# Kernel tuning notes

Hardware: AMD Instinct MI355X
Metric: run time of the kernel (lower is better)

The kernel has to match this reference:

```python
import jax, jax.numpy as jnp
import numpy as np

V, E, S_MAX, H, L = 32000, 1024, 2048, 16, 6
D = E // H  # head_dim = 64
EPS = 1e-5


def _ln(x, g, b):
    mu = jnp.mean(x, axis=-1, keepdims=True)
    var = jnp.mean(jnp.square(x - mu), axis=-1, keepdims=True)
    return (x - mu) * jax.lax.rsqrt(var + EPS) * g + b


def setup_inputs() -> dict:
    key = jax.random.key(0)
    ks = iter(jax.random.split(key, 32))
    std = 0.02
    B, S = 1, 2048
    inp = {
        "tokens": jax.random.randint(next(ks), (B, S), 0, V, dtype=jnp.int32),
        "W_emb": jax.random.normal(next(ks), (V, E), jnp.float32) * std,  # tied with fc_out
        "W_pos": jax.random.normal(next(ks), (S_MAX, E), jnp.float32) * std,
        # per-layer stacked params [L, ...]
        "Wq": jax.random.normal(next(ks), (L, E, E), jnp.float32) * std,
        "Wk": jax.random.normal(next(ks), (L, E, E), jnp.float32) * std,
        "Wv": jax.random.normal(next(ks), (L, E, E), jnp.float32) * std,
        "Wo": jax.random.normal(next(ks), (L, E, E), jnp.float32) * std,
        "bo": jnp.zeros((L, E), jnp.float32),
        "ln1_g": jnp.ones((L, E), jnp.float32),
        "ln1_b": jnp.zeros((L, E), jnp.float32),
        "ln2_g": jnp.ones((L, E), jnp.float32),
        "ln2_b": jnp.zeros((L, E), jnp.float32),
        "W1": jax.random.normal(next(ks), (L, 4 * E, E), jnp.float32) * std,
        "b1": jnp.zeros((L, 4 * E), jnp.float32),
        "W2": jax.random.normal(next(ks), (L, E, 4 * E), jnp.float32) * std,
        "b2": jnp.zeros((L, E), jnp.float32),
        "lnf_g": jnp.ones((E,), jnp.float32),
        "lnf_b": jnp.zeros((E,), jnp.float32),
    }
    return inp


def _gpt_forward(tokens, W_emb, W_pos, Wq, Wk, Wv, Wo, bo, ln1_g, ln1_b,
                 ln2_g, ln2_b, W1, b1, W2, b2, lnf_g, lnf_b):
    B, S = tokens.shape
    x = W_emb[tokens] + W_pos[:S][None, :, :]  # [B,S,E]
    causal = jnp.tril(jnp.ones((S, S), bool))  # [S,S]
    scale = 1.0 / np.sqrt(D)

    def block(x, p):
        wq, wk, wv, wo, bo_, g1, b1n, g2, b2n, w1, bf1, w2, bf2 = p
        h = _ln(x, g1, b1n)
        # torch Linear: y = x @ W.T ; split heads -> [B,H,S,D]
        def heads(w):
            return (h @ w.T).reshape(B, S, H, D).transpose(0, 2, 1, 3)
        q, k, v = heads(wq), heads(wk), heads(wv)
        scores = jnp.einsum('bhqd,bhkd->bhqk', q, k) * scale
        scores = jnp.where(causal[None, None], scores, -jnp.inf)
        attn = jax.nn.softmax(scores, axis=-1)
        o = jnp.einsum('bhqk,bhkd->bhqd', attn, v)
        o = o.transpose(0, 2, 1, 3).reshape(B, S, E)
        x = x + o @ wo.T + bo_
        h2 = _ln(x, g2, b2n)
        ff = jax.nn.gelu(h2 @ w1.T + bf1, approximate=False) @ w2.T + bf2
        return x + ff, None

    params = (Wq, Wk, Wv, Wo, bo, ln1_g, ln1_b, ln2_g, ln2_b, W1, b1, W2, b2)
    x, _ = jax.lax.scan(block, x, params)
    x = _ln(x, lnf_g, lnf_b)
    return x @ W_emb.T  # tied output projection [B,S,V]


def reference(tokens, W_emb, W_pos, Wq, Wk, Wv, Wo, bo, ln1_g, ln1_b,
              ln2_g, ln2_b, W1, b1, W2, b2, lnf_g, lnf_b):
    return _gpt_forward(tokens, W_emb, W_pos, Wq, Wk, Wv, Wo, bo, ln1_g,
                        ln1_b, ln2_g, ln2_b, W1, b1, W2, b2, lnf_g, lnf_b)
```

## Files before the change

kernel.cpp:

```cpp
#include <hip/hip_runtime.h>
#include <math.h>

#define S_LEN 2048
#define EMB 1024
#define NHEAD 16
#define HDIM 64
#define NLAYER 6
#define VOCAB 32000
#define FFDIM 4096

using f32x4 = __attribute__((ext_vector_type(4))) float;
using bf16x8 = __attribute__((ext_vector_type(8))) __bf16;
typedef unsigned short us;

static __device__ __forceinline__ unsigned short f2bf(float f) {
  union { float f; unsigned int u; } v; v.f = f;
  unsigned int r = v.u + 0x7FFFu + ((v.u >> 16) & 1u);
  return (unsigned short)(r >> 16);
}

#define GLOAD_LDS16(g, l)                                                      \
  __builtin_amdgcn_global_load_lds(                                            \
      (const __attribute__((address_space(1))) void*)(g),                      \
      (__attribute__((address_space(3))) void*)(l), 16, 0, 0)

__global__ __launch_bounds__(256) void cvt_bf16_kernel(
    const float* __restrict__ in, us* __restrict__ out, long n) {
  long i = ((long)blockIdx.x * 256 + threadIdx.x) * 8;
  if (i >= n) return;
  const float4* p = (const float4*)(in + i);
  float4 a = p[0], b = p[1];
  uint4 o;
  o.x = (unsigned)f2bf(a.x) | ((unsigned)f2bf(a.y) << 16);
  o.y = (unsigned)f2bf(a.z) | ((unsigned)f2bf(a.w) << 16);
  o.z = (unsigned)f2bf(b.x) | ((unsigned)f2bf(b.y) << 16);
  o.w = (unsigned)f2bf(b.z) | ((unsigned)f2bf(b.w) << 16);
  *(uint4*)(out + i) = o;
}

__global__ __launch_bounds__(256) void embed_kernel(
    const int* __restrict__ tok, const float* __restrict__ Wemb,
    const float* __restrict__ Wpos, float* __restrict__ x) {
  int s = blockIdx.x, t = threadIdx.x;
  int tk = tok[s];
  const float4* we = (const float4*)(Wemb + (size_t)tk * EMB);
  const float4* wp = (const float4*)(Wpos + (size_t)s * EMB);
  float4 a = we[t], b = wp[t];
  float4 o; o.x = a.x + b.x; o.y = a.y + b.y; o.z = a.z + b.z; o.w = a.w + b.w;
  ((float4*)(x + (size_t)s * EMB))[t] = o;
}

__global__ __launch_bounds__(256) void ln_kernel(
    const float* __restrict__ x, const float* __restrict__ g,
    const float* __restrict__ b, us* __restrict__ out) {
  int row = blockIdx.x, t = threadIdx.x, lane = t & 63, wave = t >> 6;
  float4 v = ((const float4*)(x + (size_t)row * EMB))[t];
  float s = v.x + v.y + v.z + v.w;
  float q = v.x * v.x + v.y * v.y + v.z * v.z + v.w * v.w;
  #pragma unroll
  for (int d = 1; d < 64; d <<= 1) { s += __shfl_xor(s, d); q += __shfl_xor(q, d); }
  __shared__ float rs[4], rq[4];
  if (lane == 0) { rs[wave] = s; rq[wave] = q; }
  __syncthreads();
  s = rs[0] + rs[1] + rs[2] + rs[3];
  q = rq[0] + rq[1] + rq[2] + rq[3];
  float mean = s * (1.0f / EMB);
  float var = q * (1.0f / EMB) - mean * mean;
  float rstd = rsqrtf(var + 1e-5f);
  float4 gg = ((const float4*)g)[t], bb = ((const float4*)b)[t];
  ushort4 o;
  o.x = f2bf((v.x - mean) * rstd * gg.x + bb.x);
  o.y = f2bf((v.y - mean) * rstd * gg.y + bb.y);
  o.z = f2bf((v.z - mean) * rstd * gg.z + bb.z);
  o.w = f2bf((v.w - mean) * rstd * gg.w + bb.w);
  ((ushort4*)(out + (size_t)row * EMB))[t] = o;
}

template <int HAS_BIAS, int HAS_RES, int DO_GELU, int OUT_BF16>
__global__ __launch_bounds__(256) void gemm_bb(
    const us* __restrict__ A, const us* __restrict__ B0,
    const us* __restrict__ B1, const us* __restrict__ B2,
    const float* __restrict__ bias, const float* __restrict__ res,
    void* C0, void* C1, void* C2, int M, int N, int K) {
  const us* B = blockIdx.z == 0 ? B0 : (blockIdx.z == 1 ? B1 : B2);
  void* C = blockIdx.z == 0 ? C0 : (blockIdx.z == 1 ? C1 : C2);
  const int nwg = gridDim.x * gridDim.y;
  int lin = blockIdx.y * gridDim.x + blockIdx.x;
  {
    const int qx = nwg >> 3, r = nwg & 7;
    const int xcd = lin & 7, idx = lin >> 3;
    lin = (xcd < r ? xcd * (qx + 1) : r * (qx + 1) + (xcd - r) * qx) + idx;
  }
  const int m0 = (lin % gridDim.x) * 128, n0 = (lin / gridDim.x) * 128;
  const int t = threadIdx.x, lane = t & 63, wave = t >> 6;
  const int wm = (wave >> 1) * 64, wn = (wave & 1) * 64;
  __shared__ __align__(16) us As[128 * 64];
  __shared__ __align__(16) us Bs[128 * 64];
  f32x4 acc[4][4] = {};
  const int kIters = K >> 6;
  const int cbase = wave * 64;
  const int myc = cbase + lane;
  for (int kt = 0; kt < kIters; ++kt) {
    const int k0 = kt << 6;
    __syncthreads();
    #pragma unroll
    for (int i = 0; i < 4; ++i) {
      const int c = myc + i * 256;
      const int row = c >> 3, col = (c & 7) * 8;
      GLOAD_LDS16(A + (size_t)(m0 + row) * K + k0 + col,
                  As + (size_t)(cbase + i * 256) * 8);
    }
    #pragma unroll
    for (int i = 0; i < 4; ++i) {
      const int c = myc + i * 256;
      const int row = c >> 3, col = (c & 7) * 8;
      GLOAD_LDS16(B + (size_t)(n0 + row) * K + k0 + col,
                  Bs + (size_t)(cbase + i * 256) * 8);
    }
    __syncthreads();
    #pragma unroll
    for (int ks = 0; ks < 2; ++ks) {
      bf16x8 af[4], bfr[4];
      #pragma unroll
      for (int i = 0; i < 4; ++i)
        af[i] = *(const bf16x8*)(As + (wm + i * 16 + (lane & 15)) * 64 + ks * 32 + (lane >> 4) * 8);
      #pragma unroll
      for (int j = 0; j < 4; ++j)
        bfr[j] = *(const bf16x8*)(Bs + (wn + j * 16 + (lane & 15)) * 64 + ks * 32 + (lane >> 4) * 8);
      #pragma unroll
      for (int i = 0; i < 4; ++i)
        #pragma unroll
        for (int j = 0; j < 4; ++j)
          acc[i][j] = __builtin_amdgcn_mfma_f32_16x16x32_bf16(af[i], bfr[j], acc[i][j], 0, 0, 0);
    }
  }
  const int r0 = (lane >> 4) * 4, cl = lane & 15;
  #pragma unroll
  for (int i = 0; i < 4; ++i) {
    #pragma unroll
    for (int j = 0; j < 4; ++j) {
      const int col = n0 + wn + j * 16 + cl;
      float bv = HAS_BIAS ? bias[col] : 0.0f;
      #pragma unroll
      for (int r = 0; r < 4; ++r) {
        const int row = m0 + wm + i * 16 + r0 + r;
        float val = acc[i][j][r] + bv;
        if (DO_GELU) val = val * 0.5f * (1.0f + erff(val * 0.70710678118f));
        if (HAS_RES) val += res[(size_t)row * N + col];
        if (OUT_BF16) ((us*)C)[(size_t)row * N + col] = f2bf(val);
        else          ((float*)C)[(size_t)row * N + col] = val;
      }
    }
  }
}

__global__ __launch_bounds__(256) void gemm_sk(
    const us* __restrict__ A, const us* __restrict__ B,
    float* __restrict__ C, int M, int N, int K, int kSlice) {
  const int z = blockIdx.z;
  const int nwg = gridDim.x * gridDim.y;
  int lin = blockIdx.y * gridDim.x + blockIdx.x;
  {
    const int qx = nwg >> 3, r = nwg & 7;
    const int xcd = lin & 7, idx = lin >> 3;
    lin = (xcd < r ? xcd * (qx + 1) : r * (qx + 1) + (xcd - r) * qx) + idx;
  }
  const int m0 = (lin % gridDim.x) * 128, n0 = (lin / gridDim.x) * 128;
  const int t = threadIdx.x, lane = t & 63, wave = t >> 6;
  const int wm = (wave >> 1) * 64, wn = (wave & 1) * 64;
  __shared__ __align__(16) us As[128 * 64];
  __shared__ __align__(16) us Bs[128 * 64];
  f32x4 acc[4][4] = {};
  const int cbase = wave * 64;
  const int myc = cbase + lane;
  const int kBeg = z * kSlice;
  const int kIters = kSlice >> 6;
  for (int kt = 0; kt < kIters; ++kt) {
    const int k0 = kBeg + (kt << 6);
    __syncthreads();
    #pragma unroll
    for (int i = 0; i < 4; ++i) {
      const int c = myc + i * 256;
      const int row = c >> 3, col = (c & 7) * 8;
      GLOAD_LDS16(A + (size_t)(m0 + row) * K + k0 + col,
                  As + (size_t)(cbase + i * 256) * 8);
    }
    #pragma unroll
    for (int i = 0; i < 4; ++i) {
      const int c = myc + i * 256;
      const int row = c >> 3, col = (c & 7) * 8;
      GLOAD_LDS16(B + (size_t)(n0 + row) * K + k0 + col,
                  Bs + (size_t)(cbase + i * 256) * 8);
    }
    __syncthreads();
    #pragma unroll
    for (int ks = 0; ks < 2; ++ks) {
      bf16x8 af[4], bfr[4];
      #pragma unroll
      for (int i = 0; i < 4; ++i)
        af[i] = *(const bf16x8*)(As + (wm + i * 16 + (lane & 15)) * 64 + ks * 32 + (lane >> 4) * 8);
      #pragma unroll
      for (int j = 0; j < 4; ++j)
        bfr[j] = *(const bf16x8*)(Bs + (wn + j * 16 + (lane & 15)) * 64 + ks * 32 + (lane >> 4) * 8);
      #pragma unroll
      for (int i = 0; i < 4; ++i)
        #pragma unroll
        for (int j = 0; j < 4; ++j)
          acc[i][j] = __builtin_amdgcn_mfma_f32_16x16x32_bf16(af[i], bfr[j], acc[i][j], 0, 0, 0);
    }
  }
  float* Cz = C + (size_t)z * M * N;
  const int r0 = (lane >> 4) * 4, cl = lane & 15;
  #pragma unroll
  for (int i = 0; i < 4; ++i)
    #pragma unroll
    for (int j = 0; j < 4; ++j) {
      const int col = n0 + wn + j * 16 + cl;
      #pragma unroll
      for (int r = 0; r < 4; ++r)
        Cz[(size_t)(m0 + wm + i * 16 + r0 + r) * N + col] = acc[i][j][r];
    }
}

template <int SK>
__global__ __launch_bounds__(256) void reduce_sk_kernel(
    float* __restrict__ x, const float* __restrict__ p,
    const float* __restrict__ bias) {
  const size_t i = ((size_t)blockIdx.x * 256 + threadIdx.x) * 4;
  const size_t plane = (size_t)S_LEN * EMB;
  float4 v = *(const float4*)(x + i);
  float4 b = *(const float4*)(bias + (i & (EMB - 1)));
  v.x += b.x; v.y += b.y; v.z += b.z; v.w += b.w;
  #pragma unroll
  for (int z = 0; z < SK; ++z) {
    float4 q = *(const float4*)(p + z * plane + i);
    v.x += q.x; v.y += q.y; v.z += q.z; v.w += q.w;
  }
  *(float4*)(x + i) = v;
}

__global__ __launch_bounds__(256) void attn_kernel(
    const us* __restrict__ qb, const us* __restrict__ kb,
    const us* __restrict__ vb, us* __restrict__ ob) {
  const int qt = gridDim.x - 1 - blockIdx.x;
  const int head = blockIdx.y;
  const int t = threadIdx.x, lane = t & 63, wave = t >> 6;
  const int hi = lane >> 4, lq = lane & 15;
  const int hd = head * HDIM;
  const int q0w = qt * 64 + wave * 16;
  __shared__ __align__(16) us Kl[64 * 64];
  __shared__ __align__(16) us Vl[64][72];
  __shared__ __align__(16) us Pl[4][16][72];
  bf16x8 qf[2];
  {
    const us* qp = qb + (size_t)(q0w + lq) * EMB + hd + hi * 8;
    qf[0] = *(const bf16x8*)qp;
    qf[1] = *(const bf16x8*)(qp + 32);
  }
  f32x4 accO[4] = {};
  float m_run = -1e30f, l_run = 0.f;
  const int vr = t >> 2, vd = (t & 3) * 16;
  const int q_g = q0w + lq;
  for (int kt = 0; kt <= qt; ++kt) {
    __syncthreads();
    #pragma unroll
    for (int i = 0; i < 2; ++i) {
      const int c = wave * 64 + lane + i * 256;
      const int row = c >> 3, j = c & 7;
      const int colE = (j * 8) ^ ((row & 7) << 3);
      GLOAD_LDS16(kb + (size_t)(kt * 64 + row) * EMB + hd + colE,
                  Kl + (size_t)(wave * 64 + i * 256) * 8);
    }
    {
      const us* vp = vb + (size_t)(kt * 64 + vr) * EMB + hd + vd;
      uint4 a = *(const uint4*)vp;
      uint4 b = *(const uint4*)(vp + 8);
      unsigned int w[8] = {a.x, a.y, a.z, a.w, b.x, b.y, b.z, b.w};
      #pragma unroll
      for (int i = 0; i < 8; ++i) {
        Vl[vd + 2 * i][vr] = (us)(w[i] & 0xffffu);
        Vl[vd + 2 * i + 1][vr] = (us)(w[i] >> 16);
      }
    }
    __syncthreads();
    f32x4 sc[4] = {};
    #pragma unroll
    for (int ks = 0; ks < 2; ++ks) {
      #pragma unroll
      for (int fn = 0; fn < 4; ++fn) {
        const int rowk = fn * 16 + lq;
        const us* kp = Kl + rowk * 64 + ((ks * 32 + hi * 8) ^ ((rowk & 7) << 3));
        sc[fn] = __builtin_amdgcn_mfma_f32_16x16x32_bf16(
            *(const bf16x8*)kp, qf[ks], sc[fn], 0, 0, 0);
      }
    }
    float pv[16];
    float pmax = -1e30f;
    #pragma unroll
    for (int fn = 0; fn < 4; ++fn)
      #pragma unroll
      for (int r = 0; r < 4; ++r) {
        const int k_g = kt * 64 + fn * 16 + hi * 4 + r;
        float sv = sc[fn][r] * 0.125f;
        if (k_g > q_g) sv = -1e30f;
        pv[fn * 4 + r] = sv;
        pmax = fmaxf(pmax, sv);
      }
    pmax = fmaxf(pmax, __shfl_xor(pmax, 16));
    pmax = fmaxf(pmax, __shfl_xor(pmax, 32));
    const float mn = fmaxf(m_run, pmax);
    const float alpha = __expf(m_run - mn);
    m_run = mn;
    float rsum = 0.f;
    #pragma unroll
    for (int i = 0; i < 16; ++i) {
      float e = __expf(pv[i] - mn);
      pv[i] = e;
      rsum += e;
    }
    rsum += __shfl_xor(rsum, 16);
    rsum += __shfl_xor(rsum, 32);
    l_run = l_run * alpha + rsum;
    float ar[4];
    #pragma unroll
    for (int r = 0; r < 4; ++r) ar[r] = __shfl(alpha, hi * 4 + r);
    #pragma unroll
    for (int df = 0; df < 4; ++df)
      #pragma unroll
      for (int r = 0; r < 4; ++r) accO[df][r] *= ar[r];
    #pragma unroll
    for (int fn = 0; fn < 4; ++fn) {
      ushort4 pk;
      pk.x = f2bf(pv[fn * 4 + 0]);
      pk.y = f2bf(pv[fn * 4 + 1]);
      pk.z = f2bf(pv[fn * 4 + 2]);
      pk.w = f2bf(pv[fn * 4 + 3]);
      *(ushort4*)&Pl[wave][lq][fn * 16 + hi * 4] = pk;
    }
    #pragma unroll
    for (int ks = 0; ks < 2; ++ks) {
      bf16x8 pf = *(const bf16x8*)&Pl[wave][lq][ks * 32 + hi * 8];
      #pragma unroll
      for (int df = 0; df < 4; ++df) {
        bf16x8 vf = *(const bf16x8*)&Vl[df * 16 + lq][ks * 32 + hi * 8];
        accO[df] = __builtin_amdgcn_mfma_f32_16x16x32_bf16(pf, vf, accO[df], 0, 0, 0);
      }
    }
  }
  float linv[4];
  #pragma unroll
  for (int r = 0; r < 4; ++r) linv[r] = 1.0f / __shfl(l_run, hi * 4 + r);
  #pragma unroll
  for (int r = 0; r < 4; ++r) {
    const int row = q0w + hi * 4 + r;
    #pragma unroll
    for (int df = 0; df < 4; ++df)
      ob[(size_t)row * EMB + hd + df * 16 + lq] = f2bf(accO[df][r] * linv[r]);
  }
}

extern "C" void kernel_launch(void* const* d_in, const int* in_sizes, int n_in,
                              void* d_out, int out_size, void* d_ws, size_t ws_size,
                              hipStream_t stream) {
  const int* tok = (const int*)d_in[0];
  const float* Wemb = (const float*)d_in[1];
  const float* Wpos = (const float*)d_in[2];
  const float* Wq = (const float*)d_in[3];
  const float* Wk = (const float*)d_in[4];
  const float* Wv = (const float*)d_in[5];
  const float* Wo = (const float*)d_in[6];
  const float* bo = (const float*)d_in[7];
  const float* ln1g = (const float*)d_in[8];
  const float* ln1b = (const float*)d_in[9];
  const float* ln2g = (const float*)d_in[10];
  const float* ln2b = (const float*)d_in[11];
  const float* W1 = (const float*)d_in[12];
  const float* b1 = (const float*)d_in[13];
  const float* W2 = (const float*)d_in[14];
  const float* b2 = (const float*)d_in[15];
  const float* lnfg = (const float*)d_in[16];
  const float* lnfb = (const float*)d_in[17];
  (void)in_sizes; (void)n_in; (void)out_size;

  const size_t MB = 1u << 20;
  char* ws = (char*)d_ws;
  float* x = (float*)ws;
  us* h  = (us*)(ws + 8 * MB);
  us* qb = (us*)(ws + 12 * MB);
  us* kb = (us*)(ws + 16 * MB);
  us* vb = (us*)(ws + 20 * MB);
  us* ob = (us*)(ws + 24 * MB);
  us* fb = (us*)(ws + 12 * MB);
  us* cWq = (us*)(ws + 28 * MB);
  us* cWk = (us*)(ws + 40 * MB);
  us* cWv = (us*)(ws + 52 * MB);
  us* cWo = (us*)(ws + 64 * MB);
  us* cW1 = (us*)(ws + 76 * MB);
  us* cW2 = (us*)(ws + 124 * MB);
  us* cWemb = (us*)(ws + 172 * MB);
  float* pbuf = (float*)(ws + 236 * MB);
  const size_t need_bf16 = 172 * MB + (size_t)VOCAB * EMB * 2;
  const bool bf16w = ws_size >= need_bf16;
  int skWo = 0, skF2 = 0;
  if (ws_size >= 236 * MB + 32 * MB)      { skWo = 2; skF2 = 4; }
  else if (ws_size >= 236 * MB + 16 * MB) { skWo = 2; skF2 = 2; }

  embed_kernel<<<dim3(S_LEN), 256, 0, stream>>>(tok, Wemb, Wpos, x);

  if (bf16w) {
    const long nE2 = (long)NLAYER * EMB * EMB;
    const long nF  = (long)NLAYER * FFDIM * EMB;
    const long nV  = (long)VOCAB * EMB;
    cvt_bf16_kernel<<<(int)(nE2 / 2048), 256, 0, stream>>>(Wq, cWq, nE2);
    cvt_bf16_kernel<<<(int)(nE2 / 2048), 256, 0, stream>>>(Wk, cWk, nE2);
    cvt_bf16_kernel<<<(int)(nE2 / 2048), 256, 0, stream>>>(Wv, cWv, nE2);
    cvt_bf16_kernel<<<(int)(nE2 / 2048), 256, 0, stream>>>(Wo, cWo, nE2);
    cvt_bf16_kernel<<<(int)(nF / 2048), 256, 0, stream>>>(W1, cW1, nF);
    cvt_bf16_kernel<<<(int)(nF / 2048), 256, 0, stream>>>(W2, cW2, nF);
    cvt_bf16_kernel<<<(int)(nV / 2048), 256, 0, stream>>>(Wemb, cWemb, nV);

    for (int l = 0; l < NLAYER; ++l) {
      const size_t wofs = (size_t)l * EMB * EMB;
      const size_t fofs = (size_t)l * FFDIM * EMB;
      ln_kernel<<<S_LEN, 256, 0, stream>>>(x, ln1g + l * EMB, ln1b + l * EMB, h);
      gemm_bb<0, 0, 0, 1><<<dim3(16, 8, 3), 256, 0, stream>>>(
          h, cWq + wofs, cWk + wofs, cWv + wofs, nullptr, nullptr,
          qb, kb, vb, S_LEN, EMB, EMB);
      attn_kernel<<<dim3(32, NHEAD), 256, 0, stream>>>(qb, kb, vb, ob);
      if (skWo == 2) {
        gemm_sk<<<dim3(16, 8, 2), 256, 0, stream>>>(
            ob, cWo + wofs, pbuf, S_LEN, EMB, EMB, EMB / 2);
        reduce_sk_kernel<2><<<2048, 256, 0, stream>>>(x, pbuf, bo + l * EMB);
      } else {
        gemm_bb<1, 1, 0, 0><<<dim3(16, 8, 1), 256, 0, stream>>>(
            ob, cWo + wofs, nullptr, nullptr, bo + l * EMB, x,
            x, nullptr, nullptr, S_LEN, EMB, EMB);
      }
      ln_kernel<<<S_LEN, 256, 0, stream>>>(x, ln2g + l * EMB, ln2b + l * EMB, h);
      gemm_bb<1, 0, 1, 1><<<dim3(16, 32, 1), 256, 0, stream>>>(
          h, cW1 + fofs, nullptr, nullptr, b1 + l * FFDIM, nullptr,
          fb, nullptr, nullptr, S_LEN, FFDIM, EMB);
      if (skF2 == 4) {
        gemm_sk<<<dim3(16, 8, 4), 256, 0, stream>>>(
            fb, cW2 + fofs, pbuf, S_LEN, EMB, FFDIM, FFDIM / 4);
        reduce_sk_kernel<4><<<2048, 256, 0, stream>>>(x, pbuf, b2 + l * EMB);
      } else if (skF2 == 2) {
        gemm_sk<<<dim3(16, 8, 2), 256, 0, stream>>>(
            fb, cW2 + fofs, pbuf, S_LEN, EMB, FFDIM, FFDIM / 2);
        reduce_sk_kernel<2><<<2048, 256, 0, stream>>>(x, pbuf, b2 + l * EMB);
      } else {
        gemm_bb<1, 1, 0, 0><<<dim3(16, 8, 1), 256, 0, stream>>>(
            fb, cW2 + fofs, nullptr, nullptr, b2 + l * EMB, x,
            x, nullptr, nullptr, S_LEN, EMB, FFDIM);
      }
    }
    ln_kernel<<<S_LEN, 256, 0, stream>>>(x, lnfg, lnfb, h);
    gemm_bb<0, 0, 0, 0><<<dim3(16, 250, 1), 256, 0, stream>>>(
        h, cWemb, nullptr, nullptr, nullptr, nullptr,
        d_out, nullptr, nullptr, S_LEN, VOCAB, EMB);
  } else {
  }
}
```

Measured before the change: 1.610 ms.

## Fuse split-K reduce with layernorm, pipeline attention, add 256-tile vocab GEMM

Merges each split-K reduction with the following layernorm in one kernel, removing a separate LN pass and a round trip of the residual. The attention kernel now double-buffers K/V tiles in LDS, pre-scales Q, skips the causal mask on off-diagonal tiles, and rescales the accumulator only when the running max grows by more than a threshold. The final vocab projection moves to a new 256x256-tile, 512-thread double-buffered GEMM. These add LDS pressure and small bf16 rounding changes from scaling Q before the product.

```diff
diff --git a/kernel.cpp b/kernel.cpp
--- a/kernel.cpp
+++ b/kernel.cpp
@@ -76,6 +76,43 @@
   ((ushort4*)(out + (size_t)row * EMB))[t] = o;
 }
 
+template <int SK>
+__global__ __launch_bounds__(256) void reduce_ln_kernel(
+    float* __restrict__ x, const float* __restrict__ p,
+    const float* __restrict__ bias, const float* __restrict__ g,
+    const float* __restrict__ b, us* __restrict__ out) {
+  int row = blockIdx.x, t = threadIdx.x, lane = t & 63, wave = t >> 6;
+  const size_t plane = (size_t)S_LEN * EMB;
+  float4 v = ((const float4*)(x + (size_t)row * EMB))[t];
+  float4 bb4 = ((const float4*)bias)[t];
+  v.x += bb4.x; v.y += bb4.y; v.z += bb4.z; v.w += bb4.w;
+  #pragma unroll
+  for (int z = 0; z < SK; ++z) {
+    float4 q4 = ((const float4*)(p + z * plane + (size_t)row * EMB))[t];
+    v.x += q4.x; v.y += q4.y; v.z += q4.z; v.w += q4.w;
+  }
+  ((float4*)(x + (size_t)row * EMB))[t] = v;
+  float s = v.x + v.y + v.z + v.w;
+  float q = v.x * v.x + v.y * v.y + v.z * v.z + v.w * v.w;
+  #pragma unroll
+  for (int d = 1; d < 64; d <<= 1) { s += __shfl_xor(s, d); q += __shfl_xor(q, d); }
+  __shared__ float rs[4], rq[4];
+  if (lane == 0) { rs[wave] = s; rq[wave] = q; }
+  __syncthreads();
+  s = rs[0] + rs[1] + rs[2] + rs[3];
+  q = rq[0] + rq[1] + rq[2] + rq[3];
+  float mean = s * (1.0f / EMB);
+  float var = q * (1.0f / EMB) - mean * mean;
+  float rstd = rsqrtf(var + 1e-5f);
+  float4 gg = ((const float4*)g)[t], lb = ((const float4*)b)[t];
+  ushort4 o;
+  o.x = f2bf((v.x - mean) * rstd * gg.x + lb.x);
+  o.y = f2bf((v.y - mean) * rstd * gg.y + lb.y);
+  o.z = f2bf((v.z - mean) * rstd * gg.z + lb.z);
+  o.w = f2bf((v.w - mean) * rstd * gg.w + lb.w);
+  ((ushort4*)(out + (size_t)row * EMB))[t] = o;
+}
+
 template <int HAS_BIAS, int HAS_RES, int DO_GELU, int OUT_BF16>
 __global__ __launch_bounds__(256) void gemm_bb(
     const us* __restrict__ A, const us* __restrict__ B0,
@@ -222,21 +259,77 @@
     }
 }
 
-template <int SK>
-__global__ __launch_bounds__(256) void reduce_sk_kernel(
-    float* __restrict__ x, const float* __restrict__ p,
-    const float* __restrict__ bias) {
-  const size_t i = ((size_t)blockIdx.x * 256 + threadIdx.x) * 4;
-  const size_t plane = (size_t)S_LEN * EMB;
-  float4 v = *(const float4*)(x + i);
-  float4 b = *(const float4*)(bias + (i & (EMB - 1)));
-  v.x += b.x; v.y += b.y; v.z += b.z; v.w += b.w;
-  #pragma unroll
-  for (int z = 0; z < SK; ++z) {
-    float4 q = *(const float4*)(p + z * plane + i);
-    v.x += q.x; v.y += q.y; v.z += q.z; v.w += q.w;
-  }
-  *(float4*)(x + i) = v;
+__global__ __launch_bounds__(512, 2) void gemm_v256(
+    const us* __restrict__ A, const us* __restrict__ B,
+    float* __restrict__ C, int M, int N, int K) {
+  const int nwg = gridDim.x * gridDim.y;
+  int lin = blockIdx.y * gridDim.x + blockIdx.x;
+  {
+    const int qx = nwg >> 3, r = nwg & 7;
+    const int xcd = lin & 7, idx = lin >> 3;
+    lin = (xcd < r ? xcd * (qx + 1) : r * (qx + 1) + (xcd - r) * qx) + idx;
+  }
+  const int m0 = (lin % gridDim.x) * 256, n0 = (lin / gridDim.x) * 256;
+  const int t = threadIdx.x, lane = t & 63, wave = t >> 6;
+  const int lq = lane & 15, hi = lane >> 4;
+  const int wm = (wave >> 2) * 128, wn = (wave & 3) * 64;
+  __shared__ __align__(16) us As[2][256 * 64];
+  __shared__ __align__(16) us Bs[2][256 * 64];
+  f32x4 acc[8][4] = {};
+  const int kIters = K >> 6;
+  const int ldsbase = (wave * 64) * 8;
+
+  {
+    const int k0 = 0;
+    #pragma unroll
+    for (int i = 0; i < 4; ++i) {
+      const int c = t + i * 512;
+      const int row = c >> 3, col = (c & 7) * 8;
+      GLOAD_LDS16(A + (size_t)(m0 + row) * K + k0 + col, &As[0][0] + ldsbase + i * 512 * 8);
+      GLOAD_LDS16(B + (size_t)(n0 + row) * K + k0 + col, &Bs[0][0] + ldsbase + i * 512 * 8);
+    }
+  }
+  __syncthreads();
+  int cur = 0;
+  for (int kt = 0; kt < kIters; ++kt) {
+    if (kt + 1 < kIters) {
+      const int k0 = (kt + 1) << 6;
+      #pragma unroll
+      for (int i = 0; i < 4; ++i) {
+        const int c = t + i * 512;
+        const int row = c >> 3, col = (c & 7) * 8;
+        GLOAD_LDS16(A + (size_t)(m0 + row) * K + k0 + col,
+                    &As[cur ^ 1][0] + ldsbase + i * 512 * 8);
+        GLOAD_LDS16(B + (size_t)(n0 + row) * K + k0 + col,
+                    &Bs[cur ^ 1][0] + ldsbase + i * 512 * 8);
+      }
+    }
+    #pragma unroll
+    for (int ks = 0; ks < 2; ++ks) {
+      bf16x8 bfr[4];
+      #pragma unroll
+      for (int j = 0; j < 4; ++j)
+        bfr[j] = *(const bf16x8*)(&Bs[cur][0] + (wn + j * 16 + lq) * 64 + ks * 32 + hi * 8);
+      #pragma unroll
+      for (int i = 0; i < 8; ++i) {
+        bf16x8 af = *(const bf16x8*)(&As[cur][0] + (wm + i * 16 + lq) * 64 + ks * 32 + hi * 8);
+        #pragma unroll
+        for (int j = 0; j < 4; ++j)
+          acc[i][j] = __builtin_amdgcn_mfma_f32_16x16x32_bf16(af, bfr[j], acc[i][j], 0, 0, 0);
+      }
+    }
+    __syncthreads();
+    cur ^= 1;
+  }
+  #pragma unroll
+  for (int i = 0; i < 8; ++i)
+    #pragma unroll
+    for (int j = 0; j < 4; ++j) {
+      const int col = n0 + wn + j * 16 + lq;
+      #pragma unroll
+      for (int r = 0; r < 4; ++r)
+        C[(size_t)(m0 + wm + i * 16 + hi * 4 + r) * N + col] = acc[i][j][r];
+    }
 }
 
 __global__ __launch_bounds__(256) void attn_kernel(
@@ -248,86 +341,122 @@
   const int hi = lane >> 4, lq = lane & 15;
   const int hd = head * HDIM;
   const int q0w = qt * 64 + wave * 16;
-  __shared__ __align__(16) us Kl[64 * 64];
-  __shared__ __align__(16) us Vl[64][72];
+  __shared__ __align__(16) us Kl[2][64 * 64];
+  __shared__ __align__(16) us Vl[2][64 * 72];
   __shared__ __align__(16) us Pl[4][16][72];
   bf16x8 qf[2];
   {
     const us* qp = qb + (size_t)(q0w + lq) * EMB + hd + hi * 8;
     qf[0] = *(const bf16x8*)qp;
     qf[1] = *(const bf16x8*)(qp + 32);
+    #pragma unroll
+    for (int e = 0; e < 8; ++e) {
+      qf[0][e] = (__bf16)((float)qf[0][e] * 0.125f);
+      qf[1][e] = (__bf16)((float)qf[1][e] * 0.125f);
+    }
   }
   f32x4 accO[4] = {};
   float m_run = -1e30f, l_run = 0.f;
-  const int vr = t >> 2, vd = (t & 3) * 16;
+  const int vr2 = (t >> 3) * 2, d8 = (t & 7) * 8;
   const int q_g = q0w + lq;
-  for (int kt = 0; kt <= qt; ++kt) {
-    __syncthreads();
+
+  {
     #pragma unroll
     for (int i = 0; i < 2; ++i) {
       const int c = wave * 64 + lane + i * 256;
       const int row = c >> 3, j = c & 7;
       const int colE = (j * 8) ^ ((row & 7) << 3);
-      GLOAD_LDS16(kb + (size_t)(kt * 64 + row) * EMB + hd + colE,
-                  Kl + (size_t)(wave * 64 + i * 256) * 8);
-    }
-    {
-      const us* vp = vb + (size_t)(kt * 64 + vr) * EMB + hd + vd;
-      uint4 a = *(const uint4*)vp;
-      uint4 b = *(const uint4*)(vp + 8);
-      unsigned int w[8] = {a.x, a.y, a.z, a.w, b.x, b.y, b.z, b.w};
-      #pragma unroll
-      for (int i = 0; i < 8; ++i) {
-        Vl[vd + 2 * i][vr] = (us)(w[i] & 0xffffu);
-        Vl[vd + 2 * i + 1][vr] = (us)(w[i] >> 16);
+      GLOAD_LDS16(kb + (size_t)(row) * EMB + hd + colE,
+                  &Kl[0][0] + (wave * 64 + i * 256) * 8);
+    }
+    const us* vp = vb + (size_t)vr2 * EMB + hd + d8;
+    uint4 vA = *(const uint4*)vp;
+    uint4 vB = *(const uint4*)(vp + EMB);
+    const unsigned* wa = (const unsigned*)&vA;
+    const unsigned* wb = (const unsigned*)&vB;
+    #pragma unroll
+    for (int i = 0; i < 8; ++i) {
+      unsigned lo = (i & 1) ? (wa[i >> 1] >> 16) : (wa[i >> 1] & 0xffffu);
+      unsigned hw = (i & 1) ? (wb[i >> 1] >> 16) : (wb[i >> 1] & 0xffffu);
+      *(unsigned*)(&Vl[0][0] + (d8 + i) * 72 + vr2) = lo | (hw << 16);
+    }
+  }
+  __syncthreads();
+  int cur = 0;
+  for (int kt = 0; kt <= qt; ++kt) {
+    uint4 vA, vB;
+    if (kt < qt) {
+      #pragma unroll
+      for (int i = 0; i < 2; ++i) {
+        const int c = wave * 64 + lane + i * 256;
+        const int row = c >> 3, j = c & 7;
+        const int colE = (j * 8) ^ ((row & 7) << 3);
+        GLOAD_LDS16(kb + (size_t)((kt + 1) * 64 + row) * EMB + hd + colE,
+                    &Kl[cur ^ 1][0] + (wave * 64 + i * 256) * 8);
       }
-    }
-    __syncthreads();
+      const us* vp = vb + (size_t)((kt + 1) * 64 + vr2) * EMB + hd + d8;
+      vA = *(const uint4*)vp;
+      vB = *(const uint4*)(vp + EMB);
+    }
     f32x4 sc[4] = {};
     #pragma unroll
     for (int ks = 0; ks < 2; ++ks) {
       #pragma unroll
       for (int fn = 0; fn < 4; ++fn) {
         const int rowk = fn * 16 + lq;
-        const us* kp = Kl + rowk * 64 + ((ks * 32 + hi * 8) ^ ((rowk & 7) << 3));
+        const us* kp = &Kl[cur][0] + rowk * 64 + ((ks * 32 + hi * 8) ^ ((rowk & 7) << 3));
         sc[fn] = __builtin_amdgcn_mfma_f32_16x16x32_bf16(
             *(const bf16x8*)kp, qf[ks], sc[fn], 0, 0, 0);
       }
     }
     float pv[16];
     float pmax = -1e30f;
-    #pragma unroll
-    for (int fn = 0; fn < 4; ++fn)
-      #pragma unroll
-      for (int r = 0; r < 4; ++r) {
-        const int k_g = kt * 64 + fn * 16 + hi * 4 + r;
-        float sv = sc[fn][r] * 0.125f;
-        if (k_g > q_g) sv = -1e30f;
-        pv[fn * 4 + r] = sv;
-        pmax = fmaxf(pmax, sv);
-      }
+    if (kt == qt) {
+      #pragma unroll
+      for (int fn = 0; fn < 4; ++fn)
+        #pragma unroll
+        for (int r = 0; r < 4; ++r) {
+          const int k_g = kt * 64 + fn * 16 + hi * 4 + r;
+          float sv = sc[fn][r];
+          if (k_g > q_g) sv = -1e30f;
+          pv[fn * 4 + r] = sv;
+          pmax = fmaxf(pmax, sv);
+        }
+    } else {
+      #pragma unroll
+      for (int fn = 0; fn < 4; ++fn)
+        #pragma unroll
+        for (int r = 0; r < 4; ++r) {
+          float sv = sc[fn][r];
+          pv[fn * 4 + r] = sv;
+          pmax = fmaxf(pmax, sv);
+        }
+    }
     pmax = fmaxf(pmax, __shfl_xor(pmax, 16));
     pmax = fmaxf(pmax, __shfl_xor(pmax, 32));
-    const float mn = fmaxf(m_run, pmax);
-    const float alpha = __expf(m_run - mn);
-    m_run = mn;
+    if (!__all(pmax <= m_run + 8.0f)) {
+      const float mn = fmaxf(m_run, pmax);
+      const float alpha = __expf(m_run - mn);
+      m_run = mn;
+      l_run *= alpha;
+      float ar[4];
+      #pragma unroll
+      for (int r = 0; r < 4; ++r) ar[r] = __shfl(alpha, hi * 4 + r);
+      #pragma unroll
+      for (int df = 0; df < 4; ++df)
+        #pragma unroll
+        for (int r = 0; r < 4; ++r) accO[df][r] *= ar[r];
+    }
     float rsum = 0.f;
     #pragma unroll
     for (int i = 0; i < 16; ++i) {
-      float e = __expf(pv[i] - mn);
+      float e = __expf(pv[i] - m_run);
       pv[i] = e;
       rsum += e;
     }
     rsum += __shfl_xor(rsum, 16);
     rsum += __shfl_xor(rsum, 32);
-    l_run = l_run * alpha + rsum;
-    float ar[4];
-    #pragma unroll
-    for (int r = 0; r < 4; ++r) ar[r] = __shfl(alpha, hi * 4 + r);
-    #pragma unroll
-    for (int df = 0; df < 4; ++df)
-      #pragma unroll
-      for (int r = 0; r < 4; ++r) accO[df][r] *= ar[r];
+    l_run += rsum;
     #pragma unroll
     for (int fn = 0; fn < 4; ++fn) {
       ushort4 pk;
@@ -342,10 +471,22 @@
       bf16x8 pf = *(const bf16x8*)&Pl[wave][lq][ks * 32 + hi * 8];
       #pragma unroll
       for (int df = 0; df < 4; ++df) {
-        bf16x8 vf = *(const bf16x8*)&Vl[df * 16 + lq][ks * 32 + hi * 8];
+        bf16x8 vf = *(const bf16x8*)(&Vl[cur][0] + (df * 16 + lq) * 72 + ks * 32 + hi * 8);
         accO[df] = __builtin_amdgcn_mfma_f32_16x16x32_bf16(pf, vf, accO[df], 0, 0, 0);
       }
     }
+    if (kt < qt) {
+      const unsigned* wa = (const unsigned*)&vA;
+      const unsigned* wb = (const unsigned*)&vB;
+      #pragma unroll
+      for (int i = 0; i < 8; ++i) {
+        unsigned lo = (i & 1) ? (wa[i >> 1] >> 16) : (wa[i >> 1] & 0xffffu);
+        unsigned hw = (i & 1) ? (wb[i >> 1] >> 16) : (wb[i >> 1] & 0xffffu);
+        *(unsigned*)(&Vl[cur ^ 1][0] + (d8 + i) * 72 + vr2) = lo | (hw << 16);
+      }
+    }
+    __syncthreads();
+    cur ^= 1;
   }
   float linv[4];
   #pragma unroll
@@ -404,60 +545,63 @@
   int skWo = 0, skF2 = 0;
   if (ws_size >= 236 * MB + 32 * MB)      { skWo = 2; skF2 = 4; }
   else if (ws_size >= 236 * MB + 16 * MB) { skWo = 2; skF2 = 2; }
+  const bool fused = (skWo == 2 && skF2 == 4);
 
   embed_kernel<<<dim3(S_LEN), 256, 0, stream>>>(tok, Wemb, Wpos, x);
-
-  if (bf16w) {
-    const long nE2 = (long)NLAYER * EMB * EMB;
-    const long nF  = (long)NLAYER * FFDIM * EMB;
-    const long nV  = (long)VOCAB * EMB;
-    cvt_bf16_kernel<<<(int)(nE2 / 2048), 256, 0, stream>>>(Wq, cWq, nE2);
-    cvt_bf16_kernel<<<(int)(nE2 / 2048), 256, 0, stream>>>(Wk, cWk, nE2);
-    cvt_bf16_kernel<<<(int)(nE2 / 2048), 256, 0, stream>>>(Wv, cWv, nE2);
-    cvt_bf16_kernel<<<(int)(nE2 / 2048), 256, 0, stream>>>(Wo, cWo, nE2);
-    cvt_bf16_kernel<<<(int)(nF / 2048), 256, 0, stream>>>(W1, cW1, nF);
-    cvt_bf16_kernel<<<(int)(nF / 2048), 256, 0, stream>>>(W2, cW2, nF);
-    cvt_bf16_kernel<<<(int)(nV / 2048), 256, 0, stream>>>(Wemb, cWemb, nV);
-
-    for (int l = 0; l < NLAYER; ++l) {
-      const size_t wofs = (size_t)l * EMB * EMB;
-      const size_t fofs = (size_t)l * FFDIM * EMB;
-      ln_kernel<<<S_LEN, 256, 0, stream>>>(x, ln1g + l * EMB, ln1b + l * EMB, h);
-      gemm_bb<0, 0, 0, 1><<<dim3(16, 8, 3), 256, 0, stream>>>(
-          h, cWq + wofs, cWk + wofs, cWv + wofs, nullptr, nullptr,
-          qb, kb, vb, S_LEN, EMB, EMB);
-      attn_kernel<<<dim3(32, NHEAD), 256, 0, stream>>>(qb, kb, vb, ob);
-      if (skWo == 2) {
-        gemm_sk<<<dim3(16, 8, 2), 256, 0, stream>>>(
-            ob, cWo + wofs, pbuf, S_LEN, EMB, EMB, EMB / 2);
-        reduce_sk_kernel<2><<<2048, 256, 0, stream>>>(x, pbuf, bo + l * EMB);
-      } else {
-        gemm_bb<1, 1, 0, 0><<<dim3(16, 8, 1), 256, 0, stream>>>(
-            ob, cWo + wofs, nullptr, nullptr, bo + l * EMB, x,
-            x, nullptr, nullptr, S_LEN, EMB, EMB);
-      }
+  if (!bf16w) return;
+
+  const long nE2 = (long)NLAYER * EMB * EMB;
+  const long nF  = (long)NLAYER * FFDIM * EMB;
+  const long nV  = (long)VOCAB * EMB;
+  cvt_bf16_kernel<<<(int)(nE2 / 2048), 256, 0, stream>>>(Wq, cWq, nE2);
+  cvt_bf16_kernel<<<(int)(nE2 / 2048), 256, 0, stream>>>(Wk, cWk, nE2);
+  cvt_bf16_kernel<<<(int)(nE2 / 2048), 256, 0, stream>>>(Wv, cWv, nE2);
+  cvt_bf16_kernel<<<(int)(nE2 / 2048), 256, 0, stream>>>(Wo, cWo, nE2);
+  cvt_bf16_kernel<<<(int)(nF / 2048), 256, 0, stream>>>(W1, cW1, nF);
+  cvt_bf16_kernel<<<(int)(nF / 2048), 256, 0, stream>>>(W2, cW2, nF);
+  cvt_bf16_kernel<<<(int)(nV / 2048), 256, 0, stream>>>(Wemb, cWemb, nV);
+
+  ln_kernel<<<S_LEN, 256, 0, stream>>>(x, ln1g, ln1b, h);
+  for (int l = 0; l < NLAYER; ++l) {
+    const size_t wofs = (size_t)l * EMB * EMB;
+    const size_t fofs = (size_t)l * FFDIM * EMB;
+    gemm_bb<0, 0, 0, 1><<<dim3(16, 8, 3), 256, 0, stream>>>(
+        h, cWq + wofs, cWk + wofs, cWv + wofs, nullptr, nullptr,
+        qb, kb, vb, S_LEN, EMB, EMB);
+    attn_kernel<<<dim3(32, NHEAD), 256, 0, stream>>>(qb, kb, vb, ob);
+    if (fused) {
+      gemm_sk<<<dim3(16, 8, 2), 256, 0, stream>>>(
+          ob, cWo + wofs, pbuf, S_LEN, EMB, EMB, EMB / 2);
+      reduce_ln_kernel<2><<<S_LEN, 256, 0, stream>>>(
+          x, pbuf, bo + l * EMB, ln2g + l * EMB, ln2b + l * EMB, h);
+      gemm_bb<1, 0, 1, 1><<<dim3(16, 32, 1), 256, 0, stream>>>(
+          h, cW1 + fofs, nullptr, nullptr, b1 + l * FFDIM, nullptr,
+          fb, nullptr, nullptr, S_LEN, FFDIM, EMB);
+      gemm_sk<<<dim3(16, 8, 4), 256, 0, stream>>>(
+          fb, cW2 + fofs, pbuf, S_LEN, EMB, FFDIM, FFDIM / 4);
+      if (l < NLAYER - 1)
+        reduce_ln_kernel<4><<<S_LEN, 256, 0, stream>>>(
+            x, pbuf, b2 + l * EMB, ln1g + (l + 1) * EMB, ln1b + (l + 1) * EMB, h);
+      else
+        reduce_ln_kernel<4><<<S_LEN, 256, 0, stream>>>(
+            x, pbuf, b2 + l * EMB, lnfg, lnfb, h);
+    } else {
+      gemm_bb<1, 1, 0, 0><<<dim3(16, 8, 1), 256, 0, stream>>>(
+          ob, cWo + wofs, nullptr, nullptr, bo + l * EMB, x,
+          x, nullptr, nullptr, S_LEN, EMB, EMB);
       ln_kernel<<<S_LEN, 256, 0, stream>>>(x, ln2g + l * EMB, ln2b + l * EMB, h);
       gemm_bb<1, 0, 1, 1><<<dim3(16, 32, 1), 256, 0, stream>>>(
           h, cW1 + fofs, nullptr, nullptr, b1 + l * FFDIM, nullptr,
           fb, nullptr, nullptr, S_LEN, FFDIM, EMB);
-      if (skF2 == 4) {
-        gemm_sk<<<dim3(16, 8, 4), 256, 0, stream>>>(
-            fb, cW2 + fofs, pbuf, S_LEN, EMB, FFDIM, FFDIM / 4);
-        reduce_sk_kernel<4><<<2048, 256, 0, stream>>>(x, pbuf, b2 + l * EMB);
-      } else if (skF2 == 2) {
-        gemm_sk<<<dim3(16, 8, 2), 256, 0, stream>>>(
-            fb, cW2 + fofs, pbuf, S_LEN, EMB, FFDIM, FFDIM / 2);
-        reduce_sk_kernel<2><<<2048, 256, 0, stream>>>(x, pbuf, b2 + l * EMB);
-      } else {
-        gemm_bb<1, 1, 0, 0><<<dim3(16, 8, 1), 256, 0, stream>>>(
-            fb, cW2 + fofs, nullptr, nullptr, b2 + l * EMB, x,
-            x, nullptr, nullptr, S_LEN, EMB, FFDIM);
-      }
-    }
-    ln_kernel<<<S_LEN, 256, 0, stream>>>(x, lnfg, lnfb, h);
-    gemm_bb<0, 0, 0, 0><<<dim3(16, 250, 1), 256, 0, stream>>>(
-        h, cWemb, nullptr, nullptr, nullptr, nullptr,
-        d_out, nullptr, nullptr, S_LEN, VOCAB, EMB);
-  } else {
-  }
-}
+      gemm_bb<1, 1, 0, 0><<<dim3(16, 8, 1), 256, 0, stream>>>(
+          fb, cW2 + fofs, nullptr, nullptr, b2 + l * EMB, x,
+          x, nullptr, nullptr, S_LEN, EMB, FFDIM);
+      if (l < NLAYER - 1)
+        ln_kernel<<<S_LEN, 256, 0, stream>>>(x, ln1g + (l + 1) * EMB, ln1b + (l + 1) * EMB, h);
+      else
+        ln_kernel<<<S_LEN, 256, 0, stream>>>(x, lnfg, lnfb, h);
+    }
+  }
+  gemm_v256<<<dim3(8, 125), 512, 0, stream>>>(
+      h, cWemb, (float*)d_out, S_LEN, VOCAB, EMB);
+}
```

Measured after the change: 1.499 ms. 6.9% less time.
